# Performance work log

Hardware: AMD Instinct MI355X
Metric: run time of the kernel (lower is better)

Reference implementation:

```python
import jax, jax.numpy as jnp
import numpy as np

B, N, F, H = 64, 1024, 128, 256  # graphs, nodes per graph, nfeat, nhid


def setup_inputs() -> dict:
    key = jax.random.key(0)
    ks = jax.random.split(key, 8)
    s_in = 1.0 / np.sqrt(F)
    s_h = 1.0 / np.sqrt(H)
    return {
        "embs": jax.random.normal(ks[0], (B, N, F), jnp.float32),
        "adjmat": jax.random.uniform(ks[1], (B, N, N), jnp.float32) / N,  # row-scaled dense adjacency
        "W0": jax.random.normal(ks[2], (F, H), jnp.float32) * s_in,
        "b0": jnp.zeros((H,), jnp.float32),
        "W1": jax.random.normal(ks[3], (H, H), jnp.float32) * s_h,
        "b1": jnp.zeros((H,), jnp.float32),
        "W2": jax.random.normal(ks[4], (H, H), jnp.float32) * s_h,
        "b2": jnp.zeros((H,), jnp.float32),
        "Wl": jax.random.normal(ks[5], (H, F), jnp.float32) * s_h,
        "bl": jnp.zeros((F,), jnp.float32),
    }


def reference(embs, adjmat, W0, b0, W1, b1, W2, b2, Wl, bl):
    # Batched form of the per-graph loop: every adj is N x N, so the
    # x[:adj.shape[0]] slice is identity and all graphs fuse into one GEMM.
    hid = embs  # [B, N, F]
    for W, b in ((W0, b0), (W1, b1), (W2, b2)):
        # GraphConvolution: adj @ (x @ W) + b, then relu
        hid = jax.nn.relu(jnp.einsum('bnm,bmh->bnh', adjmat, hid @ W) + b)
    out = hid @ Wl + bl          # [B, N, F] linear_hid
    return out[:, 0, :]          # hid[0] per graph -> [B, F]
```

## Files before the change

kernel.cpp:

```cpp
#include <hip/hip_runtime.h>
#include <stdint.h>

typedef __bf16 bf16;
typedef __bf16 bf16x8 __attribute__((ext_vector_type(8)));
typedef float f32x4 __attribute__((ext_vector_type(4)));

enum { EPI_STORE = 0, EPI_BIAS_RELU = 1, EPI_VRED = 2 };

__device__ __forceinline__ void gload16(const bf16* g, bf16* l) {
  __builtin_amdgcn_global_load_lds(
      (const __attribute__((address_space(1))) unsigned int*)g,
      (__attribute__((address_space(3))) unsigned int*)l, 16, 0, 0);
}

template<bool A_F32, int EPI>
__global__ __launch_bounds__(256, 2)
void gemm_bt(const void* __restrict__ Ap, const bf16* __restrict__ Btp,
             const float* __restrict__ bias, bf16* __restrict__ C,
             float* __restrict__ vpart, const float* __restrict__ adjp,
             int K, int ldA, int ldBt, int ldC,
             long sA, long sBt, long sC)
{
  constexpr int BM = 128, BN = 256, BK = 32;
  __shared__ __align__(16) char raw[73728];
  auto Asb = [&](int b) -> bf16* { return (bf16*)(raw + b * 8192); };
  auto Bsb = [&](int b) -> bf16* { return (bf16*)(raw + 24576 + b * 16384); };
  __shared__ float a0s[BM];
  __shared__ float vsum[BN];

  const int tid  = threadIdx.x;
  const int lane = tid & 63;
  const int wid  = tid >> 6;
  const int wm   = wid >> 1;
  const int wn   = wid & 1;
  const int l15  = lane & 15;
  const int quad = lane >> 4;

  const int nb = blockIdx.x, mb = blockIdx.y, g = blockIdx.z;

  const long aoff = (long)g * sA + (long)mb * BM * ldA;
  const long boff = (long)g * sBt + (long)nb * BN * ldBt;

  if constexpr (EPI == EPI_VRED) {
    if (tid < BM) a0s[tid] = adjp[(long)g * sA + mb * BM + tid];
    vsum[tid] = 0.f;
  }

  const int r   = tid >> 2;
  const int c4  = tid & 3;
  const int sw  = (r >> 1) & 3;
  const int kcs = (c4 ^ sw) << 3;
  const int kcp = c4 << 3;
  const int csw = (quad ^ ((l15 >> 1) & 3)) << 3;

  const int n  = K / BK;
  const int nm = n - 1;
  const int off = (g * 11 + mb * 5 + nb * 3) & nm;
  auto kof = [&](int s) { return ((s + off) & nm) * BK; };

  const bf16* Bg0 = Btp + boff;

  auto issueB = [&](int k0, int buf) {
    const bf16* Bg = Bg0 + k0;
    #pragma unroll
    for (int p = 0; p < 4; ++p)
      gload16(Bg + (long)(p * 64 + r) * ldBt + kcs, Bsb(buf) + p * 2048 + tid * 8);
  };
  auto issueAg = [&](int k0, int buf) {
    const bf16* Ag = (const bf16*)Ap + aoff + k0;
    #pragma unroll
    for (int p = 0; p < 2; ++p)
      gload16(Ag + (long)(p * 64 + r) * ldA + kcs, Asb(buf) + p * 2048 + tid * 8);
  };
  auto issueAf = [&](int k0, f32x4 (&pf)[4]) {
    const float* Ag = (const float*)Ap + aoff + k0;
    #pragma unroll
    for (int p = 0; p < 2; ++p) {
      const f32x4* src = (const f32x4*)(Ag + (long)(p * 64 + r) * ldA + kcp);
      pf[p * 2 + 0] = __builtin_nontemporal_load(src);
      pf[p * 2 + 1] = __builtin_nontemporal_load(src + 1);
    }
  };
  auto commitAf = [&](f32x4 (&pf)[4], int buf) {
    #pragma unroll
    for (int p = 0; p < 2; ++p) {
      f32x4 v0 = pf[p * 2 + 0], v1 = pf[p * 2 + 1];
      bf16x8 w;
      w[0]=(bf16)v0[0]; w[1]=(bf16)v0[1]; w[2]=(bf16)v0[2]; w[3]=(bf16)v0[3];
      w[4]=(bf16)v1[0]; w[5]=(bf16)v1[1]; w[6]=(bf16)v1[2]; w[7]=(bf16)v1[3];
      *(bf16x8*)(Asb(buf) + p * 2048 + r * 32 + kcs) = w;
    }
  };

  f32x4 acc[4][8] = {};

  if constexpr (!A_F32) {
    issueAg(kof(0), 0); issueB(kof(0), 0);
    if (n > 1) { issueAg(kof(1), 1); issueB(kof(1), 1); }
    for (int s = 0; s < n; ++s) {
      const int b = s % 3;
      if (s + 2 < n) { issueAg(kof(s + 2), (s + 2) % 3); issueB(kof(s + 2), (s + 2) % 3); }
      if (s + 2 < n)      asm volatile("s_waitcnt vmcnt(12)" ::: "memory");
      else if (s + 1 < n) asm volatile("s_waitcnt vmcnt(6)"  ::: "memory");
      else                asm volatile("s_waitcnt vmcnt(0)"  ::: "memory");
      __builtin_amdgcn_s_barrier();

      bf16x8 af[4], bfr[8];
      #pragma unroll
      for (int i = 0; i < 4; ++i)
        af[i] = *(const bf16x8*)(Asb(b) + (wm * 64 + i * 16 + l15) * 32 + csw);
      #pragma unroll
      for (int j = 0; j < 8; ++j)
        bfr[j] = *(const bf16x8*)(Bsb(b) + (wn * 128 + j * 16 + l15) * 32 + csw);
      asm volatile("s_waitcnt lgkmcnt(0)" ::: "memory");
      __builtin_amdgcn_s_barrier();

      #pragma unroll
      for (int i = 0; i < 4; ++i)
        #pragma unroll
        for (int j = 0; j < 8; ++j)
          acc[i][j] = __builtin_amdgcn_mfma_f32_16x16x32_bf16(af[i], bfr[j], acc[i][j], 0, 0, 0);
    }
  } else {
    f32x4 pfa[4], pfb[4];
    issueAf(kof(0), pfa); issueB(kof(0), 0);
    issueAf(kof(1), pfb); issueB(kof(1), 1);
    commitAf(pfa, 0);
    asm volatile("s_waitcnt vmcnt(8)" ::: "memory");
    asm volatile("s_waitcnt lgkmcnt(0)" ::: "memory");
    __builtin_amdgcn_s_barrier();

    auto bodyF = [&](int s, f32x4 (&pfI)[4], f32x4 (&pfC)[4]) {
      const int b = s % 3;
      if (s + 2 < n) { issueAf(kof(s + 2), pfI); issueB(kof(s + 2), (s + 2) % 3); }
      if (s + 2 < n)      asm volatile("s_waitcnt vmcnt(16)" ::: "memory");
      else if (s + 1 < n) asm volatile("s_waitcnt vmcnt(8)"  ::: "memory");
      else                asm volatile("s_waitcnt vmcnt(0)"  ::: "memory");
      __builtin_amdgcn_s_barrier();

      bf16x8 af[4], bfr[8];
      #pragma unroll
      for (int i = 0; i < 4; ++i)
        af[i] = *(const bf16x8*)(Asb(b) + (wm * 64 + i * 16 + l15) * 32 + csw);
      #pragma unroll
      for (int j = 0; j < 8; ++j)
        bfr[j] = *(const bf16x8*)(Bsb(b) + (wn * 128 + j * 16 + l15) * 32 + csw);
      if (s + 1 < n) commitAf(pfC, (s + 1) % 3);
      asm volatile("s_waitcnt lgkmcnt(0)" ::: "memory");
      __builtin_amdgcn_s_barrier();

      #pragma unroll
      for (int i = 0; i < 4; ++i)
        #pragma unroll
        for (int j = 0; j < 8; ++j)
          acc[i][j] = __builtin_amdgcn_mfma_f32_16x16x32_bf16(af[i], bfr[j], acc[i][j], 0, 0, 0);
    };
    for (int s = 0; s < n; s += 2) { bodyF(s, pfa, pfb); bodyF(s + 1, pfb, pfa); }
  }

  if constexpr (EPI == EPI_STORE || EPI == EPI_BIAS_RELU) {
    constexpr int LDW = 140;
    bf16* slab = (bf16*)(raw + wid * 17920);
    #pragma unroll
    for (int j = 0; j < 8; ++j) {
      float bv = 0.f;
      if constexpr (EPI == EPI_BIAS_RELU) bv = bias[nb * BN + wn * 128 + j * 16 + l15];
      #pragma unroll
      for (int i = 0; i < 4; ++i)
        #pragma unroll
        for (int rr = 0; rr < 4; ++rr) {
          float v = acc[i][j][rr];
          if constexpr (EPI == EPI_BIAS_RELU) v = fmaxf(v + bv, 0.f);
          slab[(i * 16 + quad * 4 + rr) * LDW + j * 16 + l15] = (bf16)v;
        }
    }
    asm volatile("s_waitcnt lgkmcnt(0)" ::: "memory");
    bf16* Cg = C + (long)g * sC + (long)(mb * BM + wm * 64) * ldC + nb * BN + wn * 128;
    #pragma unroll
    for (int t = 0; t < 16; ++t) {
      const int rowl = t * 4 + quad;
      bf16x8 w = *(const bf16x8*)&slab[rowl * LDW + l15 * 8];
      *(bf16x8*)&Cg[(long)rowl * ldC + l15 * 8] = w;
    }
  } else {
    __syncthreads();
    #pragma unroll
    for (int j = 0; j < 8; ++j) {
      const int col = wn * 128 + j * 16 + l15;
      const float bv = bias[col];
      float p = 0.f;
      #pragma unroll
      for (int i = 0; i < 4; ++i) {
        const int lr = wm * 64 + i * 16 + quad * 4;
        #pragma unroll
        for (int rr = 0; rr < 4; ++rr)
          p += fmaxf(acc[i][j][rr] + bv, 0.f) * a0s[lr + rr];
      }
      atomicAdd(&vsum[col], p);
    }
    __syncthreads();
    vpart[((long)g * 8 + mb) * 256 + tid] = vsum[tid];
  }
}

__global__ void cvt1(const float* __restrict__ src, bf16* __restrict__ dst, long n8)
{
  const long stride = (long)gridDim.x * blockDim.x;
  for (long i = (long)blockIdx.x * blockDim.x + threadIdx.x; i < n8; i += stride) {
    const f32x4* s = (const f32x4*)(src + i * 8);
    f32x4 v0 = s[0], v1 = s[1];
    bf16x8 w;
    w[0]=(bf16)v0[0]; w[1]=(bf16)v0[1]; w[2]=(bf16)v0[2]; w[3]=(bf16)v0[3];
    w[4]=(bf16)v1[0]; w[5]=(bf16)v1[1]; w[6]=(bf16)v1[2]; w[7]=(bf16)v1[3];
    *(bf16x8*)(dst + i * 8) = w;
  }
}

__global__ void prep_w(const float* __restrict__ W0, const float* __restrict__ W1,
                       bf16* __restrict__ W0t, bf16* __restrict__ W1t)
{
  const int idx = blockIdx.x * 256 + threadIdx.x;
  if (idx < 256 * 128) {
    const int h = idx >> 7, k = idx & 127;
    W0t[idx] = (bf16)W0[k * 256 + h];
  }
  const int h = idx >> 8, k = idx & 255;
  W1t[idx] = (bf16)W1[k * 256 + h];
}

__global__ void finish_k(const float* __restrict__ vpart, const float* __restrict__ W2,
                         const float* __restrict__ b2, const float* __restrict__ Wl,
                         const float* __restrict__ bl, float* __restrict__ out)
{
  const int b = blockIdx.x, t = threadIdx.x;
  __shared__ float v[256], h3[256];
  float s = 0.f;
  #pragma unroll
  for (int mb = 0; mb < 8; ++mb) s += vpart[((long)b * 8 + mb) * 256 + t];
  v[t] = s;
  __syncthreads();
  float z = b2[t];
  for (int k = 0; k < 256; ++k) z += v[k] * W2[k * 256 + t];
  h3[t] = fmaxf(z, 0.f);
  __syncthreads();
  if (t < 128) {
    float o = bl[t];
    for (int h = 0; h < 256; ++h) o += h3[h] * Wl[h * 128 + t];
    out[(long)b * 128 + t] = o;
  }
}

extern "C" void kernel_launch(void* const* d_in, const int* in_sizes, int n_in,
                              void* d_out, int out_size, void* d_ws, size_t ws_size,
                              hipStream_t stream) {
  const float* embs = (const float*)d_in[0];
  const float* adj  = (const float*)d_in[1];
  const float* W0   = (const float*)d_in[2];
  const float* b0   = (const float*)d_in[3];
  const float* W1   = (const float*)d_in[4];
  const float* b1   = (const float*)d_in[5];
  const float* W2   = (const float*)d_in[6];
  const float* b2   = (const float*)d_in[7];
  const float* Wl   = (const float*)d_in[8];
  const float* bl   = (const float*)d_in[9];
  float* out = (float*)d_out;

  char* ws = (char*)d_ws;
  bf16*  Zt     = (bf16*)(ws);
  bf16*  Hb     = (bf16*)(ws + 33554432);
  bf16*  W0t    = (bf16*)(ws + 67108864);
  bf16*  W1t    = (bf16*)(ws + 67174400);
  float* vpart  = (float*)(ws + 67305472);
  bf16*  embs16 = (bf16*)(ws + 67829760);

  prep_w<<<256, 256, 0, stream>>>(W0, W1, W0t, W1t);
  cvt1<<<2048, 256, 0, stream>>>(embs, embs16, 64L * 1024 * 128 / 8);

  gemm_bt<false, EPI_STORE><<<dim3(4, 2, 64), 256, 0, stream>>>(
      W0t, embs16, nullptr, Zt, nullptr, nullptr,
      128, 128, 128, 1024, 0L, 131072L, 262144L);

  gemm_bt<true, EPI_BIAS_RELU><<<dim3(1, 8, 64), 256, 0, stream>>>(
      adj, Zt, b0, Hb, nullptr, nullptr,
      1024, 1024, 1024, 256, 1048576L, 262144L, 262144L);

  gemm_bt<false, EPI_STORE><<<dim3(4, 2, 64), 256, 0, stream>>>(
      W1t, Hb, nullptr, Zt, nullptr, nullptr,
      256, 256, 256, 1024, 0L, 262144L, 262144L);

  gemm_bt<true, EPI_VRED><<<dim3(1, 8, 64), 256, 0, stream>>>(
      adj, Zt, b1, nullptr, vpart, adj,
      1024, 1024, 1024, 256, 1048576L, 262144L, 0L);

  finish_k<<<64, 256, 0, stream>>>(vpart, W2, b2, Wl, bl, out);
}
```

Baseline: 550.8 us.

## Shrink GEMM tiles to 64x128 with double buffering and higher occupancy

Every GEMM now uses 64x128 output tiles instead of 128x256, with 2 LDS buffers instead of 3. LDS use drops and launch bounds allow 4 blocks per CU, so grids become larger. The adjacency GEMMs now split the hidden dimension across two blocks, so each fp32 adjacency row block is fetched twice, possibly served from cache. The per-block partial row sums are widened to 16 row blocks, and the final reduction and workspace layout are adjusted to match. The trade is more parallelism and latency hiding against lower reuse per tile, more redundant adjacency traffic and a shallower prefetch pipeline.

```diff
diff --git a/kernel.cpp b/kernel.cpp
--- a/kernel.cpp
+++ b/kernel.cpp
@@ -14,17 +14,17 @@
 }
 
 template<bool A_F32, int EPI>
-__global__ __launch_bounds__(256, 2)
+__global__ __launch_bounds__(256, 4)
 void gemm_bt(const void* __restrict__ Ap, const bf16* __restrict__ Btp,
              const float* __restrict__ bias, bf16* __restrict__ C,
              float* __restrict__ vpart, const float* __restrict__ adjp,
              int K, int ldA, int ldBt, int ldC,
              long sA, long sBt, long sC)
 {
-  constexpr int BM = 128, BN = 256, BK = 32;
-  __shared__ __align__(16) char raw[73728];
-  auto Asb = [&](int b) -> bf16* { return (bf16*)(raw + b * 8192); };
-  auto Bsb = [&](int b) -> bf16* { return (bf16*)(raw + 24576 + b * 16384); };
+  constexpr int BM = 64, BN = 128, BK = 32;
+  __shared__ __align__(16) char raw[24576];
+  auto Asb = [&](int b) -> bf16* { return (bf16*)(raw + b * 4096); };
+  auto Bsb = [&](int b) -> bf16* { return (bf16*)(raw + 8192 + b * 8192); };
   __shared__ float a0s[BM];
   __shared__ float vsum[BN];
 
@@ -43,7 +43,7 @@
 
   if constexpr (EPI == EPI_VRED) {
     if (tid < BM) a0s[tid] = adjp[(long)g * sA + mb * BM + tid];
-    vsum[tid] = 0.f;
+    if (tid < BN) vsum[tid] = 0.f;
   }
 
   const int r   = tid >> 2;
@@ -63,110 +63,101 @@
   auto issueB = [&](int k0, int buf) {
     const bf16* Bg = Bg0 + k0;
     #pragma unroll
-    for (int p = 0; p < 4; ++p)
+    for (int p = 0; p < 2; ++p)
       gload16(Bg + (long)(p * 64 + r) * ldBt + kcs, Bsb(buf) + p * 2048 + tid * 8);
   };
   auto issueAg = [&](int k0, int buf) {
     const bf16* Ag = (const bf16*)Ap + aoff + k0;
-    #pragma unroll
-    for (int p = 0; p < 2; ++p)
-      gload16(Ag + (long)(p * 64 + r) * ldA + kcs, Asb(buf) + p * 2048 + tid * 8);
-  };
-  auto issueAf = [&](int k0, f32x4 (&pf)[4]) {
+    gload16(Ag + (long)r * ldA + kcs, Asb(buf) + tid * 8);
+  };
+  auto issueAf = [&](int k0, f32x4 (&pf)[2]) {
     const float* Ag = (const float*)Ap + aoff + k0;
-    #pragma unroll
-    for (int p = 0; p < 2; ++p) {
-      const f32x4* src = (const f32x4*)(Ag + (long)(p * 64 + r) * ldA + kcp);
-      pf[p * 2 + 0] = __builtin_nontemporal_load(src);
-      pf[p * 2 + 1] = __builtin_nontemporal_load(src + 1);
-    }
-  };
-  auto commitAf = [&](f32x4 (&pf)[4], int buf) {
-    #pragma unroll
-    for (int p = 0; p < 2; ++p) {
-      f32x4 v0 = pf[p * 2 + 0], v1 = pf[p * 2 + 1];
-      bf16x8 w;
-      w[0]=(bf16)v0[0]; w[1]=(bf16)v0[1]; w[2]=(bf16)v0[2]; w[3]=(bf16)v0[3];
-      w[4]=(bf16)v1[0]; w[5]=(bf16)v1[1]; w[6]=(bf16)v1[2]; w[7]=(bf16)v1[3];
-      *(bf16x8*)(Asb(buf) + p * 2048 + r * 32 + kcs) = w;
-    }
-  };
-
-  f32x4 acc[4][8] = {};
+    const f32x4* src = (const f32x4*)(Ag + (long)r * ldA + kcp);
+    pf[0] = __builtin_nontemporal_load(src);
+    pf[1] = __builtin_nontemporal_load(src + 1);
+  };
+  auto commitAf = [&](f32x4 (&pf)[2], int buf) {
+    f32x4 v0 = pf[0], v1 = pf[1];
+    bf16x8 w;
+    w[0]=(bf16)v0[0]; w[1]=(bf16)v0[1]; w[2]=(bf16)v0[2]; w[3]=(bf16)v0[3];
+    w[4]=(bf16)v1[0]; w[5]=(bf16)v1[1]; w[6]=(bf16)v1[2]; w[7]=(bf16)v1[3];
+    *(bf16x8*)(Asb(buf) + r * 32 + kcs) = w;
+  };
+
+  f32x4 acc[2][4] = {};
 
   if constexpr (!A_F32) {
     issueAg(kof(0), 0); issueB(kof(0), 0);
-    if (n > 1) { issueAg(kof(1), 1); issueB(kof(1), 1); }
     for (int s = 0; s < n; ++s) {
-      const int b = s % 3;
-      if (s + 2 < n) { issueAg(kof(s + 2), (s + 2) % 3); issueB(kof(s + 2), (s + 2) % 3); }
-      if (s + 2 < n)      asm volatile("s_waitcnt vmcnt(12)" ::: "memory");
-      else if (s + 1 < n) asm volatile("s_waitcnt vmcnt(6)"  ::: "memory");
-      else                asm volatile("s_waitcnt vmcnt(0)"  ::: "memory");
-      __builtin_amdgcn_s_barrier();
-
-      bf16x8 af[4], bfr[8];
-      #pragma unroll
-      for (int i = 0; i < 4; ++i)
-        af[i] = *(const bf16x8*)(Asb(b) + (wm * 64 + i * 16 + l15) * 32 + csw);
-      #pragma unroll
-      for (int j = 0; j < 8; ++j)
-        bfr[j] = *(const bf16x8*)(Bsb(b) + (wn * 128 + j * 16 + l15) * 32 + csw);
+      const int b = s & 1;
+      if (s + 1 < n) { issueAg(kof(s + 1), b ^ 1); issueB(kof(s + 1), b ^ 1); }
+      if (s + 1 < n) asm volatile("s_waitcnt vmcnt(3)" ::: "memory");
+      else           asm volatile("s_waitcnt vmcnt(0)" ::: "memory");
+      __builtin_amdgcn_s_barrier();
+
+      bf16x8 af[2], bfr[4];
+      #pragma unroll
+      for (int i = 0; i < 2; ++i)
+        af[i] = *(const bf16x8*)(Asb(b) + (wm * 32 + i * 16 + l15) * 32 + csw);
+      #pragma unroll
+      for (int j = 0; j < 4; ++j)
+        bfr[j] = *(const bf16x8*)(Bsb(b) + (wn * 64 + j * 16 + l15) * 32 + csw);
       asm volatile("s_waitcnt lgkmcnt(0)" ::: "memory");
       __builtin_amdgcn_s_barrier();
 
       #pragma unroll
-      for (int i = 0; i < 4; ++i)
-        #pragma unroll
-        for (int j = 0; j < 8; ++j)
+      for (int i = 0; i < 2; ++i)
+        #pragma unroll
+        for (int j = 0; j < 4; ++j)
           acc[i][j] = __builtin_amdgcn_mfma_f32_16x16x32_bf16(af[i], bfr[j], acc[i][j], 0, 0, 0);
     }
   } else {
-    f32x4 pfa[4], pfb[4];
+    f32x4 pfa[2], pfb[2];
     issueAf(kof(0), pfa); issueB(kof(0), 0);
-    issueAf(kof(1), pfb); issueB(kof(1), 1);
+    issueAf(kof(1), pfb);
     commitAf(pfa, 0);
-    asm volatile("s_waitcnt vmcnt(8)" ::: "memory");
+    asm volatile("s_waitcnt vmcnt(2)" ::: "memory");
     asm volatile("s_waitcnt lgkmcnt(0)" ::: "memory");
     __builtin_amdgcn_s_barrier();
 
-    auto bodyF = [&](int s, f32x4 (&pfI)[4], f32x4 (&pfC)[4]) {
-      const int b = s % 3;
-      if (s + 2 < n) { issueAf(kof(s + 2), pfI); issueB(kof(s + 2), (s + 2) % 3); }
-      if (s + 2 < n)      asm volatile("s_waitcnt vmcnt(16)" ::: "memory");
-      else if (s + 1 < n) asm volatile("s_waitcnt vmcnt(8)"  ::: "memory");
-      else                asm volatile("s_waitcnt vmcnt(0)"  ::: "memory");
-      __builtin_amdgcn_s_barrier();
-
-      bf16x8 af[4], bfr[8];
-      #pragma unroll
-      for (int i = 0; i < 4; ++i)
-        af[i] = *(const bf16x8*)(Asb(b) + (wm * 64 + i * 16 + l15) * 32 + csw);
-      #pragma unroll
-      for (int j = 0; j < 8; ++j)
-        bfr[j] = *(const bf16x8*)(Bsb(b) + (wn * 128 + j * 16 + l15) * 32 + csw);
-      if (s + 1 < n) commitAf(pfC, (s + 1) % 3);
+    auto bodyF = [&](int s, f32x4 (&pfI)[2], f32x4 (&pfC)[2]) {
+      const int b = s & 1;
+      if (s + 2 < n) issueAf(kof(s + 2), pfI);
+      if (s + 1 < n) issueB(kof(s + 1), b ^ 1);
+      if (s + 2 < n)      asm volatile("s_waitcnt vmcnt(4)" ::: "memory");
+      else if (s + 1 < n) asm volatile("s_waitcnt vmcnt(2)" ::: "memory");
+      else                asm volatile("s_waitcnt vmcnt(0)" ::: "memory");
+      __builtin_amdgcn_s_barrier();
+
+      bf16x8 af[2], bfr[4];
+      #pragma unroll
+      for (int i = 0; i < 2; ++i)
+        af[i] = *(const bf16x8*)(Asb(b) + (wm * 32 + i * 16 + l15) * 32 + csw);
+      #pragma unroll
+      for (int j = 0; j < 4; ++j)
+        bfr[j] = *(const bf16x8*)(Bsb(b) + (wn * 64 + j * 16 + l15) * 32 + csw);
+      if (s + 1 < n) commitAf(pfC, b ^ 1);
       asm volatile("s_waitcnt lgkmcnt(0)" ::: "memory");
       __builtin_amdgcn_s_barrier();
 
       #pragma unroll
-      for (int i = 0; i < 4; ++i)
-        #pragma unroll
-        for (int j = 0; j < 8; ++j)
+      for (int i = 0; i < 2; ++i)
+        #pragma unroll
+        for (int j = 0; j < 4; ++j)
           acc[i][j] = __builtin_amdgcn_mfma_f32_16x16x32_bf16(af[i], bfr[j], acc[i][j], 0, 0, 0);
     };
     for (int s = 0; s < n; s += 2) { bodyF(s, pfa, pfb); bodyF(s + 1, pfb, pfa); }
   }
 
   if constexpr (EPI == EPI_STORE || EPI == EPI_BIAS_RELU) {
-    constexpr int LDW = 140;
-    bf16* slab = (bf16*)(raw + wid * 17920);
-    #pragma unroll
-    for (int j = 0; j < 8; ++j) {
+    constexpr int LDW = 80;
+    bf16* slab = (bf16*)(raw + wid * 5120);
+    #pragma unroll
+    for (int j = 0; j < 4; ++j) {
       float bv = 0.f;
-      if constexpr (EPI == EPI_BIAS_RELU) bv = bias[nb * BN + wn * 128 + j * 16 + l15];
-      #pragma unroll
-      for (int i = 0; i < 4; ++i)
+      if constexpr (EPI == EPI_BIAS_RELU) bv = bias[nb * BN + wn * 64 + j * 16 + l15];
+      #pragma unroll
+      for (int i = 0; i < 2; ++i)
         #pragma unroll
         for (int rr = 0; rr < 4; ++rr) {
           float v = acc[i][j][rr];
@@ -175,23 +166,24 @@
         }
     }
     asm volatile("s_waitcnt lgkmcnt(0)" ::: "memory");
-    bf16* Cg = C + (long)g * sC + (long)(mb * BM + wm * 64) * ldC + nb * BN + wn * 128;
-    #pragma unroll
-    for (int t = 0; t < 16; ++t) {
-      const int rowl = t * 4 + quad;
-      bf16x8 w = *(const bf16x8*)&slab[rowl * LDW + l15 * 8];
-      *(bf16x8*)&Cg[(long)rowl * ldC + l15 * 8] = w;
+    bf16* Cg = C + (long)g * sC + (long)(mb * BM + wm * 32) * ldC + nb * BN + wn * 64;
+    #pragma unroll
+    for (int t = 0; t < 4; ++t) {
+      const int rowl = t * 8 + (lane >> 3);
+      const int c8 = lane & 7;
+      bf16x8 w = *(const bf16x8*)&slab[rowl * LDW + c8 * 8];
+      *(bf16x8*)&Cg[(long)rowl * ldC + c8 * 8] = w;
     }
   } else {
     __syncthreads();
     #pragma unroll
-    for (int j = 0; j < 8; ++j) {
-      const int col = wn * 128 + j * 16 + l15;
+    for (int j = 0; j < 4; ++j) {
+      const int col = wn * 64 + j * 16 + l15;
       const float bv = bias[col];
       float p = 0.f;
       #pragma unroll
-      for (int i = 0; i < 4; ++i) {
-        const int lr = wm * 64 + i * 16 + quad * 4;
+      for (int i = 0; i < 2; ++i) {
+        const int lr = wm * 32 + i * 16 + quad * 4;
         #pragma unroll
         for (int rr = 0; rr < 4; ++rr)
           p += fmaxf(acc[i][j][rr] + bv, 0.f) * a0s[lr + rr];
@@ -199,7 +191,8 @@
       atomicAdd(&vsum[col], p);
     }
     __syncthreads();
-    vpart[((long)g * 8 + mb) * 256 + tid] = vsum[tid];
+    if (tid < BN)
+      vpart[((long)g * 16 + mb) * 256 + nb * BN + tid] = vsum[tid];
   }
 }
 
@@ -236,7 +229,7 @@
   __shared__ float v[256], h3[256];
   float s = 0.f;
   #pragma unroll
-  for (int mb = 0; mb < 8; ++mb) s += vpart[((long)b * 8 + mb) * 256 + t];
+  for (int mb = 0; mb < 16; ++mb) s += vpart[((long)b * 16 + mb) * 256 + t];
   v[t] = s;
   __syncthreads();
   float z = b2[t];
@@ -271,24 +264,24 @@
   bf16*  W0t    = (bf16*)(ws + 67108864);
   bf16*  W1t    = (bf16*)(ws + 67174400);
   float* vpart  = (float*)(ws + 67305472);
-  bf16*  embs16 = (bf16*)(ws + 67829760);
+  bf16*  embs16 = (bf16*)(ws + 100663296);
 
   prep_w<<<256, 256, 0, stream>>>(W0, W1, W0t, W1t);
   cvt1<<<2048, 256, 0, stream>>>(embs, embs16, 64L * 1024 * 128 / 8);
 
-  gemm_bt<false, EPI_STORE><<<dim3(4, 2, 64), 256, 0, stream>>>(
+  gemm_bt<false, EPI_STORE><<<dim3(8, 4, 64), 256, 0, stream>>>(
       W0t, embs16, nullptr, Zt, nullptr, nullptr,
       128, 128, 128, 1024, 0L, 131072L, 262144L);
 
-  gemm_bt<true, EPI_BIAS_RELU><<<dim3(1, 8, 64), 256, 0, stream>>>(
+  gemm_bt<true, EPI_BIAS_RELU><<<dim3(2, 16, 64), 256, 0, stream>>>(
       adj, Zt, b0, Hb, nullptr, nullptr,
       1024, 1024, 1024, 256, 1048576L, 262144L, 262144L);
 
-  gemm_bt<false, EPI_STORE><<<dim3(4, 2, 64), 256, 0, stream>>>(
+  gemm_bt<false, EPI_STORE><<<dim3(8, 4, 64), 256, 0, stream>>>(
       W1t, Hb, nullptr, Zt, nullptr, nullptr,
       256, 256, 256, 1024, 0L, 262144L, 262144L);
 
-  gemm_bt<true, EPI_VRED><<<dim3(1, 8, 64), 256, 0, stream>>>(
+  gemm_bt<true, EPI_VRED><<<dim3(2, 16, 64), 256, 0, stream>>>(
       adj, Zt, b1, nullptr, vpart, adj,
       1024, 1024, 1024, 256, 1048576L, 262144L, 0L);
 
```

Measured after the change: 690.1 us. +25.3%, slower.
